# Kernel tuning notes

Hardware: AMD Instinct MI355X
Metric: run time of the kernel (lower is better)

## Reference

```python
import jax, jax.numpy as jnp
import numpy as np

MODES = 16

def setup_inputs() -> dict:
    key = jax.random.key(0)
    k1, k2 = jax.random.split(key)
    x = jax.random.normal(k1, (16, 32, 256, 256), dtype=jnp.float32)
    weights = jax.random.normal(k2, (32, 32, MODES, MODES, 2), dtype=jnp.float32) * 0.1
    return {"x": x, "weights": weights}

def reference(x, weights):
    # x: [B, Ci, H, W]; weights: [Ci, Co, m, m, 2]
    B, Ci, H, W = x.shape
    m = weights.shape[2]
    Co = weights.shape[1]
    x_ft = jnp.fft.rfft2(x, axes=(-2, -1))  # [B, Ci, H, W//2+1] complex
    w_c = jax.lax.complex(weights[..., 0], weights[..., 1])  # [Ci, Co, m, m]
    low = jnp.einsum('bixy,ioxy->boxy', x_ft[:, :, :m, :m], w_c)  # [B, Co, m, m]
    out_ft = jnp.zeros((B, Co, H, W // 2 + 1), dtype=x_ft.dtype)
    out_ft = out_ft.at[:, :, :m, :m].set(low)
    return jnp.fft.irfft2(out_ft, s=(H, W), axes=(-2, -1)).astype(x.dtype)
```

## Files before the change

### kernel.cpp

```cpp
#include <hip/hip_runtime.h>

typedef float v4 __attribute__((ext_vector_type(4)));

#define TWO_PI_256 0.024543692606170259f


__global__ __launch_bounds__(256) void k1_dftw(const float* __restrict__ x,
                                               float* __restrict__ F) {
  __shared__ float2 tbl[256];
  __shared__ float T[32][264];
  __shared__ float Xs[32][132];
  const int tid = threadIdx.x;
  {
    float sv, cv;
    sincosf((float)tid * TWO_PI_256, &sv, &cv);
    tbl[tid] = make_float2(cv, sv);
  }
  __syncthreads();
#pragma unroll
  for (int kx = 0; kx < 16; ++kx) {
    const float2 v = tbl[(kx * tid) & 255];
    T[2 * kx][tid] = v.x;
    T[2 * kx + 1][tid] = -v.y;
  }
  const int cg = tid & 7;
  const int rg = tid >> 3;
  const int o0 = cg * 4;
  const int r0 = rg * 4;
  const long rblk = (long)blockIdx.x * 128;
  float acc[4][4] = {};
  for (int kc = 0; kc < 256; kc += 32) {
    __syncthreads();
#pragma unroll
    for (int p = 0; p < 4; ++p) {
      const int row = (tid >> 3) + p * 32;
      const int k4 = (tid & 7) * 4;
      const v4 v = *(const v4*)&x[(rblk + row) * 256 + kc + k4];
      Xs[k4 + 0][row] = v[0];
      Xs[k4 + 1][row] = v[1];
      Xs[k4 + 2][row] = v[2];
      Xs[k4 + 3][row] = v[3];
    }
    __syncthreads();
#pragma unroll
    for (int k = 0; k < 32; k += 4) {
      v4 xv[4], tv[4];
#pragma unroll
      for (int i = 0; i < 4; ++i) xv[i] = *(const v4*)&Xs[k + i][r0];
#pragma unroll
      for (int c = 0; c < 4; ++c) tv[c] = *(const v4*)&T[o0 + c][kc + k];
#pragma unroll
      for (int i = 0; i < 4; ++i)
#pragma unroll
        for (int r = 0; r < 4; ++r)
#pragma unroll
          for (int c = 0; c < 4; ++c) acc[r][c] += xv[i][r] * tv[c][i];
    }
  }
#pragma unroll
  for (int r = 0; r < 4; ++r) {
    v4 o;
#pragma unroll
    for (int c = 0; c < 4; ++c) o[c] = acc[r][c];
    *(v4*)&F[(rblk + r0 + r) * 32 + o0] = o;
  }
}

__global__ __launch_bounds__(256) void k2_dfth(const float* __restrict__ F,
                                               float* __restrict__ X) {
  __shared__ float2 tbl[256];
  __shared__ float Fs[64][36];
  const int tid = threadIdx.x;
  const int bc = blockIdx.x;
  {
    float sv, cv;
    sincosf((float)tid * TWO_PI_256, &sv, &cv);
    tbl[tid] = make_float2(cv, sv);
  }
  const int kx = tid & 15;
  const int ky = tid >> 4;
  float xr = 0.f, xi = 0.f;
  const float* Fb = F + (long)bc * 8192;
  for (int hc = 0; hc < 256; hc += 64) {
    __syncthreads();
#pragma unroll
    for (int p = 0; p < 2; ++p) {
      const int h = (tid >> 3) + p * 32;
      const int j = (tid & 7) * 4;
      *(v4*)&Fs[h][j] = *(const v4*)&Fb[(hc + h) * 32 + j];
    }
    __syncthreads();
#pragma unroll 8
    for (int hl = 0; hl < 64; ++hl) {
      const int h = hc + hl;
      const float2 f = *(const float2*)&Fs[hl][2 * kx];
      const float2 w = tbl[(ky * h) & 255];
      xr += f.x * w.x + f.y * w.y;
      xi += f.y * w.x - f.x * w.y;
    }
  }
  *(float2*)&X[((long)bc * 256 + tid) * 2] = make_float2(xr, xi);
}

__global__ __launch_bounds__(256) void k3_mix(const float* __restrict__ X,
                                              const float* __restrict__ Wt,
                                              float* __restrict__ Y) {
  const int t = threadIdx.x;
  const int co = blockIdx.x;
  const int b = blockIdx.y;
  float yr = 0.f, yi = 0.f;
#pragma unroll 4
  for (int ci = 0; ci < 32; ++ci) {
    const float2 xv = *(const float2*)&X[((long)(b * 32 + ci) * 256 + t) * 2];
    const float2 wv = *(const float2*)&Wt[((long)(ci * 32 + co) * 256 + t) * 2];
    yr += xv.x * wv.x - xv.y * wv.y;
    yi += xv.x * wv.y + xv.y * wv.x;
  }
  *(float2*)&Y[((long)(b * 32 + co) * 256 + t) * 2] = make_float2(yr, yi);
}

__global__ __launch_bounds__(256) void k4_inv(const float* __restrict__ Y,
                                              float* __restrict__ out) {
  __shared__ float2 tbl[256];
  __shared__ float2 Ys[256];
  __shared__ float G[256][36];
  const int tid = threadIdx.x;
  const int co = blockIdx.x;
  const int b = blockIdx.y;
  {
    float sv, cv;
    sincosf((float)tid * TWO_PI_256, &sv, &cv);
    tbl[tid] = make_float2(cv, sv);
  }
  Ys[tid] = *(const float2*)&Y[((long)(b * 32 + co) * 256 + tid) * 2];
  __syncthreads();
  {
    float gr[16] = {}, gi[16] = {};
#pragma unroll 4
    for (int ky = 0; ky < 16; ++ky) {
      const float2 w = tbl[(ky * tid) & 255];
#pragma unroll
      for (int kx = 0; kx < 16; ++kx) {
        const float2 yv = Ys[ky * 16 + kx];
        gr[kx] += yv.x * w.x - yv.y * w.y;
        gi[kx] += yv.x * w.y + yv.y * w.x;
      }
    }
#pragma unroll
    for (int kx = 0; kx < 16; ++kx)
      *(float2*)&G[tid][2 * kx] = make_float2(gr[kx], gi[kx]);
  }
  __syncthreads();
  const int s = tid & 127;
  const int hh = tid >> 7;
  float cs[16], sn[16];
#pragma unroll
  for (int kx = 1; kx < 16; ++kx) {
    const float2 w = tbl[(kx * s) & 255];
    cs[kx] = 2.f * w.x;
    sn[kx] = 2.f * w.y;
  }
  const float inv = 1.f / 65536.f;
  float* __restrict__ ob = out + (long)(b * 32 + co) * 65536;
  for (int h = hh; h < 256; h += 2) {
    float gr[16], gi[16];
#pragma unroll
    for (int j = 0; j < 8; ++j) {
      const v4 q = *(const v4*)&G[h][4 * j];
      gr[2 * j] = q[0];
      gi[2 * j] = q[1];
      gr[2 * j + 1] = q[2];
      gi[2 * j + 1] = q[3];
    }
    float a = gr[0];
    float bs = 0.f;
#pragma unroll
    for (int kx = 1; kx < 16; ++kx) {
      a += gr[kx] * cs[kx];
      bs += gi[kx] * sn[kx];
    }
    if (s == 0) {
      float a128 = gr[0];
#pragma unroll
      for (int kx = 1; kx < 16; ++kx)
        a128 += (kx & 1) ? -2.f * gr[kx] : 2.f * gr[kx];
      ob[h * 256] = a * inv;
      ob[h * 256 + 128] = a128 * inv;
    } else {
      ob[h * 256 + s] = (a - bs) * inv;
      ob[h * 256 + 256 - s] = (a + bs) * inv;
    }
  }
}

extern "C" void kernel_launch(void* const* d_in, const int* in_sizes, int n_in,
                              void* d_out, int out_size, void* d_ws, size_t ws_size,
                              hipStream_t stream) {
  const float* x = (const float*)d_in[0];
  const float* wt = (const float*)d_in[1];
  float* out = (float*)d_out;
  float* F = (float*)d_ws;
  float* X = F + 4194304;
  float* Yv = X + 262144;
  k1_dftw<<<1024, 256, 0, stream>>>(x, F);
  k2_dfth<<<512, 256, 0, stream>>>(F, X);
  k3_mix<<<dim3(32, 16), 256, 0, stream>>>(X, wt, Yv);
  k4_inv<<<dim3(32, 16), 256, 0, stream>>>(Yv, out);
}
```

Before: 308.2 us.

## Precompute DFT twiddle table in global memory and stream tiles into LDS

Adds a tiny kernel that writes the 256x32 W-direction twiddle matrix to workspace once per call. The first DFT kernel no longer builds a full 32x264 table in LDS with sincos per block. Instead each k-chunk loads a 32x32 twiddle tile straight into LDS with global_load_lds, laid out k-major to match the Xs reads. This cuts LDS usage, which together with launch_bounds(256,4) allows more resident blocks, and removes per-block trig setup. The cost is an extra kernel launch and extra global traffic for the table.

```diff
diff --git a/kernel.cpp b/kernel.cpp
--- a/kernel.cpp
+++ b/kernel.cpp
@@ -5,24 +5,26 @@
 #define TWO_PI_256 0.024543692606170259f
 
 
-__global__ __launch_bounds__(256) void k1_dftw(const float* __restrict__ x,
-                                               float* __restrict__ F) {
-  __shared__ float2 tbl[256];
-  __shared__ float T[32][264];
+__global__ __launch_bounds__(256) void k0_trig(float* __restrict__ Tg) {
+  const int k = threadIdx.x;
+#pragma unroll
+  for (int kx = 0; kx < 16; ++kx) {
+    float sv, cv;
+    sincosf((float)((kx * k) & 255) * TWO_PI_256, &sv, &cv);
+    Tg[k * 32 + 2 * kx] = cv;
+    Tg[k * 32 + 2 * kx + 1] = -sv;
+  }
+}
+
+typedef __attribute__((address_space(1))) const unsigned int gas_u32;
+typedef __attribute__((address_space(3))) unsigned int las_u32;
+
+__global__ __launch_bounds__(256, 4) void k1_dftw(const float* __restrict__ x,
+                                                  const float* __restrict__ Tg,
+                                                  float* __restrict__ F) {
+  __shared__ float Ts[32][32];
   __shared__ float Xs[32][132];
   const int tid = threadIdx.x;
-  {
-    float sv, cv;
-    sincosf((float)tid * TWO_PI_256, &sv, &cv);
-    tbl[tid] = make_float2(cv, sv);
-  }
-  __syncthreads();
-#pragma unroll
-  for (int kx = 0; kx < 16; ++kx) {
-    const float2 v = tbl[(kx * tid) & 255];
-    T[2 * kx][tid] = v.x;
-    T[2 * kx + 1][tid] = -v.y;
-  }
   const int cg = tid & 7;
   const int rg = tid >> 3;
   const int o0 = cg * 4;
@@ -31,6 +33,9 @@
   float acc[4][4] = {};
   for (int kc = 0; kc < 256; kc += 32) {
     __syncthreads();
+    __builtin_amdgcn_global_load_lds(
+        (gas_u32*)(Tg + kc * 32 + tid * 4),
+        (las_u32*)((unsigned int*)&Ts[0][0] + (tid >> 6) * 256), 16, 0, 0);
 #pragma unroll
     for (int p = 0; p < 4; ++p) {
       const int row = (tid >> 3) + p * 32;
@@ -48,13 +53,13 @@
 #pragma unroll
       for (int i = 0; i < 4; ++i) xv[i] = *(const v4*)&Xs[k + i][r0];
 #pragma unroll
-      for (int c = 0; c < 4; ++c) tv[c] = *(const v4*)&T[o0 + c][kc + k];
+      for (int i = 0; i < 4; ++i) tv[i] = *(const v4*)&Ts[k + i][o0];
 #pragma unroll
       for (int i = 0; i < 4; ++i)
 #pragma unroll
         for (int r = 0; r < 4; ++r)
 #pragma unroll
-          for (int c = 0; c < 4; ++c) acc[r][c] += xv[i][r] * tv[c][i];
+          for (int c = 0; c < 4; ++c) acc[r][c] += xv[i][r] * tv[i][c];
     }
   }
 #pragma unroll
@@ -202,7 +207,9 @@
   float* F = (float*)d_ws;
   float* X = F + 4194304;
   float* Yv = X + 262144;
-  k1_dftw<<<1024, 256, 0, stream>>>(x, F);
+  float* Tg = Yv + 262144;
+  k0_trig<<<1, 256, 0, stream>>>(Tg);
+  k1_dftw<<<1024, 256, 0, stream>>>(x, Tg, F);
   k2_dfth<<<512, 256, 0, stream>>>(F, X);
   k3_mix<<<dim3(32, 16), 256, 0, stream>>>(X, wt, Yv);
   k4_inv<<<dim3(32, 16), 256, 0, stream>>>(Yv, out);
```

Result: faster. 297.3 us (-3.6%).
